# Kernel tuning notes

Measured on AMD Instinct MI355X. Metric: run time of the kernel, lower is better.

The kernel has to match this reference:

```python
import jax, jax.numpy as jnp
import numpy as np

NUM_FEATURES = 512
NUM_HEADS = 8
DIM_PER_HEAD = NUM_FEATURES // NUM_HEADS


def setup_inputs() -> dict:
    key = jax.random.key(0)
    ks = jax.random.split(key, 9)
    B, C, H, W = 8, NUM_FEATURES, 32, 32
    # xavier_uniform bound for 1x1 conv: sqrt(6/(fan_in+fan_out)) = sqrt(6/(2C))
    bound = float(np.sqrt(6.0 / (2.0 * C)))
    # conv bias default init: U(-1/sqrt(fan_in), 1/sqrt(fan_in))
    bbound = float(1.0 / np.sqrt(C))
    return {
        "query": jax.random.normal(ks[0], (B, C, H, W), jnp.float32),
        "key": jax.random.normal(ks[1], (B, C, H, W), jnp.float32),
        "value": jax.random.normal(ks[2], (B, C, H, W), jnp.float32),
        "wq": jax.random.uniform(ks[3], (C, C), jnp.float32, -bound, bound),
        "bq": jax.random.uniform(ks[4], (C,), jnp.float32, -bbound, bbound),
        "wk": jax.random.uniform(ks[5], (C, C), jnp.float32, -bound, bound),
        "bk": jax.random.uniform(ks[6], (C,), jnp.float32, -bbound, bbound),
        "wv": jax.random.uniform(ks[7], (C, C), jnp.float32, -bound, bound),
        "bv": jax.random.uniform(ks[8], (C,), jnp.float32, -bbound, bbound),
    }


def _proj(x, w, b):
    # 1x1 conv == per-pixel linear over channels. x: [B,C,H,W], w: [Cout,Cin]
    return jnp.einsum('oi,bihw->bohw', w, x) + b[None, :, None, None]


def _split_heads(x, nh, d):
    B, C, H, W = x.shape
    # view (B, nh, d, H*W) then permute -> (B, nh, S, d)
    return x.reshape(B, nh, d, H * W).transpose(0, 1, 3, 2)


def reference(query, key, value, wq, bq, wk, bk, wv, bv):
    B, C, H, W = query.shape
    nh, d = NUM_HEADS, DIM_PER_HEAD
    q = _split_heads(_proj(query, wq, bq), nh, d)   # [B,nh,S,d]
    k = _split_heads(_proj(key, wk, bk), nh, d)
    v = _split_heads(_proj(value, wv, bv), nh, d)
    scores = jnp.einsum('bhsd,bhtd->bhst', q, k) / jnp.sqrt(jnp.float32(d))
    attn = jax.nn.softmax(scores, axis=-1)          # [B,nh,S,S]
    out = jnp.einsum('bhst,bhtd->bhsd', attn, v)    # [B,nh,S,d]
    # combine_heads (faithful to torch): permute to (B,S,nh,d), flat reshape
    out = out.transpose(0, 2, 1, 3)                 # [B,S,nh,d]
    return out.reshape(B, C, H, W)
```

## Files before the change

kernel.cpp:

```cpp
#include <hip/hip_runtime.h>
#include <hip/hip_bf16.h>
#include <stdint.h>


typedef __attribute__((ext_vector_type(4))) float f32x4;
typedef __attribute__((ext_vector_type(8))) short short8;
typedef __attribute__((ext_vector_type(4))) unsigned int u32x4;

#define GLB_AS(p) ((const __attribute__((address_space(1))) void*)(p))
#define LDS_AS(p) ((__attribute__((address_space(3))) void*)(p))

__device__ __forceinline__ unsigned short f2b(float f) {
  unsigned int x = __builtin_bit_cast(unsigned int, f);
  x = (x + 0x7FFFu + ((x >> 16) & 1u)) >> 16;
  return (unsigned short)x;
}

__device__ __forceinline__ float exp2_hw(float x) {
  float r;
  asm("v_exp_f32 %0, %1" : "=v"(r) : "v"(x));
  return r;
}

__device__ __forceinline__ unsigned int cvtpk(float lo, float hi) {
  unsigned int r;
  asm("v_cvt_pk_bf16_f32 %0, %1, %2" : "=v"(r) : "v"(lo), "v"(hi));
  return r;
}

__device__ __forceinline__ f32x4 mfma16(short8 a, short8 b, f32x4 c) {
  return __builtin_amdgcn_mfma_f32_16x16x32_bf16(a, b, c, 0, 0, 0);
}

__global__ __launch_bounds__(256) void transpose_cast3(const float* __restrict__ Xq,
                                                       const float* __restrict__ Xk,
                                                       const float* __restrict__ Xv,
                                                       unsigned short* __restrict__ Xt) {
  __shared__ float t[64][65];
  const int which = blockIdx.z >> 3, bb = blockIdx.z & 7;
  const float* X = (which == 0) ? Xq : ((which == 1) ? Xk : Xv);
  const int s0 = blockIdx.x * 64, c0 = blockIdx.y * 64;
  const float* Xb = X + (long)bb * 512 * 1024;
  const int tid = threadIdx.x;
  const int col4 = (tid & 15) * 4;
  const int r0 = tid >> 4;
#pragma unroll
  for (int it = 0; it < 4; ++it) {
    int r = r0 + it * 16;
    const float4 v = *(const float4*)&Xb[(long)(c0 + r) * 1024 + s0 + col4];
    t[r][col4 + 0] = v.x; t[r][col4 + 1] = v.y; t[r][col4 + 2] = v.z; t[r][col4 + 3] = v.w;
  }
  __syncthreads();
  const int s = tid >> 2;
  const int cp = (tid & 3) * 16;
  unsigned int u[8];
#pragma unroll
  for (int i = 0; i < 8; ++i) {
    unsigned int lo = f2b(t[cp + 2 * i][s]);
    unsigned int hi = f2b(t[cp + 2 * i + 1][s]);
    u[i] = lo | (hi << 16);
  }
  unsigned short* dst = Xt + (long)which * 8 * 1024 * 512 +
                        ((long)bb * 1024 + s0 + s) * 512 + c0 + cp;
  ((uint4*)dst)[0] = make_uint4(u[0], u[1], u[2], u[3]);
  ((uint4*)dst)[1] = make_uint4(u[4], u[5], u[6], u[7]);
}

__global__ __launch_bounds__(256) void cast_w3(const float* __restrict__ wq,
                                               const float* __restrict__ wk,
                                               const float* __restrict__ wv,
                                               unsigned short* __restrict__ O) {
  const int y = blockIdx.y;
  const float* W = (y == 0) ? wq : ((y == 1) ? wk : wv);
  int i = blockIdx.x * 256 + threadIdx.x;
  float4 v = ((const float4*)W)[i];
  uint2 u;
  u.x = (unsigned)f2b(v.x) | ((unsigned)f2b(v.y) << 16);
  u.y = (unsigned)f2b(v.z) | ((unsigned)f2b(v.w) << 16);
  ((uint2*)(O + (long)y * 262144))[i] = u;
}

__global__ __launch_bounds__(256, 2) void gemm_proj(
    const unsigned short* __restrict__ XT, const unsigned short* __restrict__ W3,
    unsigned short* __restrict__ QKV, const float* __restrict__ bq,
    const float* __restrict__ bk, const float* __restrict__ bv) {
  __shared__ __align__(16) unsigned short lA[128 * 64];
  __shared__ __align__(16) unsigned short lB[128 * 64];
  const long SC = 1024L * 512;
  const int bid = blockIdx.x;
  const int kind = bid >> 8;
  const int rr = bid & 255;
  const int batch = rr >> 5, tile = rr & 31;
  const unsigned short *Ab, *Bb;
  unsigned short* Cb;
  const float* bias;
  int m0, n0, N, biasN;
  float scale = 1.0f;
  if (kind < 2) {
    m0 = (tile >> 2) * 128; n0 = (tile & 3) * 128; N = 512; biasN = 1;
    Ab = XT + ((long)kind * 8 + batch) * SC;
    Bb = W3 + (long)kind * 262144;
    Cb = QKV + ((long)kind * 8 + batch) * SC;
    bias = kind ? bk : bq;
    if (kind == 0) scale = 0.18033688011112042f;
  } else {
    m0 = (tile >> 3) * 128; n0 = (tile & 7) * 128; N = 1024; biasN = 0;
    Ab = W3 + 2 * 262144;
    Bb = XT + (16L + batch) * SC;
    Cb = QKV + (16L + batch) * SC;
    bias = bv;
  }
  const int tid = threadIdx.x, lane = tid & 63, wid = tid >> 6;
  const int wr = wid >> 1, wc = wid & 1;
  const int lm = lane & 15, lg = lane >> 4;
  f32x4 acc[4][4] = {};
  for (int k0 = 0; k0 < 512; k0 += 64) {
#pragma unroll
    for (int ch = wid; ch < 16; ch += 4) {
      int e = ch * 512 + lane * 8;
      int r = e >> 6, cc = e & 63;
      __builtin_amdgcn_global_load_lds(GLB_AS(Ab + (long)(m0 + r) * 512 + k0 + cc),
                                       LDS_AS(lA + ch * 512), 16, 0, 0);
      __builtin_amdgcn_global_load_lds(GLB_AS(Bb + (long)(n0 + r) * 512 + k0 + cc),
                                       LDS_AS(lB + ch * 512), 16, 0, 0);
    }
    __syncthreads();
#pragma unroll
    for (int kk = 0; kk < 2; ++kk) {
      short8 af[4], bf[4];
#pragma unroll
      for (int i = 0; i < 4; ++i)
        af[i] = *(const short8*)&lA[(wr * 64 + i * 16 + lm) * 64 + kk * 32 + 8 * lg];
#pragma unroll
      for (int j = 0; j < 4; ++j)
        bf[j] = *(const short8*)&lB[(wc * 64 + j * 16 + lm) * 64 + kk * 32 + 8 * lg];
#pragma unroll
      for (int i = 0; i < 4; ++i)
#pragma unroll
        for (int j = 0; j < 4; ++j)
          acc[i][j] = mfma16(af[i], bf[j], acc[i][j]);
    }
    __syncthreads();
  }
#pragma unroll
  for (int i = 0; i < 4; ++i)
#pragma unroll
    for (int j = 0; j < 4; ++j)
#pragma unroll
      for (int r = 0; r < 4; ++r) {
        int m = m0 + wr * 64 + i * 16 + lg * 4 + r;
        int n = n0 + wc * 64 + j * 16 + lm;
        float bvv = biasN ? bias[n] : bias[m];
        Cb[(long)m * N + n] = f2b((acc[i][j][r] + bvv) * scale);
      }
}

__global__ __launch_bounds__(256, 2) void attn(
    const unsigned short* __restrict__ Qt, const unsigned short* __restrict__ Kt,
    const unsigned short* __restrict__ V, float* __restrict__ Out) {
  __shared__ __align__(16) unsigned short lK[2][64 * 64];
  __shared__ __align__(16) unsigned short lV[2][64 * 64];
  const int flat = blockIdx.x;
  const int xcd = flat & 7, j = flat >> 3;
  const int pair = xcd * 8 + (j >> 3);
  const int st = j & 7;
  const int b = pair >> 3, h = pair & 7;
  const int tid = threadIdx.x, lane = tid & 63, w = tid >> 6;
  const int lm = lane & 15, lg = lane >> 4;
  const int s0 = st * 128 + w * 32;
  const unsigned short* Qb = Qt + ((long)b * 1024 + s0) * 512 + h * 64;
  const unsigned short* Kb = Kt + (long)b * 1024 * 512 + h * 64;
  const unsigned short* Vb = V + ((long)b * 512 + h * 64) * 1024;

  const int srow = (w << 1) * 8 + (lane >> 3);
  const int scol = ((lane & 7) ^ (lane >> 3)) * 8;
  auto stage = [&](int buf, int t0) {
#pragma unroll
    for (int jj = 0; jj < 2; ++jj) {
      int ch = (w << 1) + jj;
      int row = srow + jj * 8;
      __builtin_amdgcn_global_load_lds(GLB_AS(Kb + (long)(t0 + row) * 512 + scol),
                                       LDS_AS(&lK[buf][ch * 512]), 16, 0, 0);
      __builtin_amdgcn_global_load_lds(GLB_AS(Vb + (long)row * 1024 + t0 + scol),
                                       LDS_AS(&lV[buf][ch * 512]), 16, 0, 0);
    }
  };

  short8 qf[2][2];
#pragma unroll
  for (int si = 0; si < 2; ++si)
#pragma unroll
    for (int kk = 0; kk < 2; ++kk)
      qf[si][kk] = *(const short8*)&Qb[(si * 16 + lm) * 512 + kk * 32 + 8 * lg];

  f32x4 o[2][4] = {};
  float lsum[2] = {};

  stage(0, 0);
  __syncthreads();

#pragma unroll 1
  for (int t = 0; t < 16; ++t) {
    const int cur = t & 1;
    if (t < 15) stage(cur ^ 1, (t + 1) * 64);
    f32x4 s[2][4] = {};
    __builtin_amdgcn_s_setprio(1);
#pragma unroll
    for (int tj = 0; tj < 4; ++tj) {
      short8 kf0 = *(const short8*)&lK[cur][(tj * 16 + lm) * 64 + 8 * (lg ^ (lm & 7))];
      short8 kf1 = *(const short8*)&lK[cur][(tj * 16 + lm) * 64 + 8 * ((lg + 4) ^ (lm & 7))];
#pragma unroll
      for (int si = 0; si < 2; ++si) {
        s[si][tj] = mfma16(kf0, qf[si][0], s[si][tj]);
        s[si][tj] = mfma16(kf1, qf[si][1], s[si][tj]);
      }
    }
    __builtin_amdgcn_s_setprio(0);
#pragma unroll
    for (int si = 0; si < 2; ++si)
#pragma unroll
      for (int tj = 0; tj < 4; ++tj)
#pragma unroll
        for (int r = 0; r < 4; ++r) {
          float p = exp2_hw(s[si][tj][r]);
          s[si][tj][r] = p;
          lsum[si] += p;
        }
#pragma unroll
    for (int tk = 0; tk < 2; ++tk) {
      short8 pa[2];
#pragma unroll
      for (int si = 0; si < 2; ++si) {
        unsigned int X01 = cvtpk(s[si][2 * tk][0], s[si][2 * tk][1]);
        unsigned int X23 = cvtpk(s[si][2 * tk][2], s[si][2 * tk][3]);
        unsigned int Y01 = cvtpk(s[si][2 * tk + 1][0], s[si][2 * tk + 1][1]);
        unsigned int Y23 = cvtpk(s[si][2 * tk + 1][2], s[si][2 * tk + 1][3]);
        asm("v_permlane32_swap_b32 %0, %1" : "+v"(X01), "+v"(Y01));
        asm("v_permlane32_swap_b32 %0, %1" : "+v"(X23), "+v"(Y23));
        unsigned int Xs01 = (unsigned)__builtin_amdgcn_ds_swizzle((int)X01, 0x401F);
        unsigned int Xs23 = (unsigned)__builtin_amdgcn_ds_swizzle((int)X23, 0x401F);
        unsigned int Ys01 = (unsigned)__builtin_amdgcn_ds_swizzle((int)Y01, 0x401F);
        unsigned int Ys23 = (unsigned)__builtin_amdgcn_ds_swizzle((int)Y23, 0x401F);
        const bool b0 = (lane >> 4) & 1;
        u32x4 pw;
        pw[0] = b0 ? Ys01 : X01;
        pw[1] = b0 ? Ys23 : X23;
        pw[2] = b0 ? Y01 : Xs01;
        pw[3] = b0 ? Y23 : Xs23;
        pa[si] = __builtin_bit_cast(short8, pw);
      }
      __builtin_amdgcn_s_setprio(1);
#pragma unroll
      for (int dj = 0; dj < 4; ++dj) {
        short8 vf = *(const short8*)&lV[cur][(dj * 16 + lm) * 64 + 8 * ((tk * 4 + lg) ^ (lm & 7))];
        o[0][dj] = mfma16(pa[0], vf, o[0][dj]);
        o[1][dj] = mfma16(pa[1], vf, o[1][dj]);
      }
      __builtin_amdgcn_s_setprio(0);
    }
    __syncthreads();
  }

  float inv[2][4];
#pragma unroll
  for (int si = 0; si < 2; ++si) {
    float rs = lsum[si];
    rs += __shfl_xor(rs, 16);
    rs += __shfl_xor(rs, 32);
#pragma unroll
    for (int r = 0; r < 4; ++r)
      inv[si][r] = 1.0f / __shfl(rs, lg * 4 + r);
  }
#pragma unroll
  for (int si = 0; si < 2; ++si)
#pragma unroll
    for (int dj = 0; dj < 4; ++dj)
#pragma unroll
      for (int r = 0; r < 4; ++r) {
        int srow2 = s0 + si * 16 + lg * 4 + r;
        Out[((long)b * 1024 + srow2) * 512 + h * 64 + dj * 16 + lm] = o[si][dj][r] * inv[si][r];
      }
}

extern "C" void kernel_launch(void* const* d_in, const int* in_sizes, int n_in,
                              void* d_out, int out_size, void* d_ws, size_t ws_size,
                              hipStream_t stream) {
  const float* query = (const float*)d_in[0];
  const float* key   = (const float*)d_in[1];
  const float* value = (const float*)d_in[2];
  const float* wq = (const float*)d_in[3];
  const float* bq = (const float*)d_in[4];
  const float* wk = (const float*)d_in[5];
  const float* bk = (const float*)d_in[6];
  const float* wv = (const float*)d_in[7];
  const float* bv = (const float*)d_in[8];

  unsigned short* ws = (unsigned short*)d_ws;
  const long SC = 1024L * 512;
  unsigned short* XT  = ws;
  unsigned short* W3  = XT + 24 * SC;
  unsigned short* QKV = W3 + 3 * 262144;
  unsigned short* QT  = QKV;
  unsigned short* KTm = QKV + 8 * SC;
  unsigned short* VVm = QKV + 16 * SC;

  transpose_cast3<<<dim3(16, 8, 24), 256, 0, stream>>>(query, key, value, XT);
  cast_w3<<<dim3(256, 3), 256, 0, stream>>>(wq, wk, wv, W3);
  gemm_proj<<<768, 256, 0, stream>>>(XT, W3, QKV, bq, bk, bv);
  attn<<<512, 256, 0, stream>>>(QT, KTm, VVm, (float*)d_out);
}
```

Baseline: 69.40 us.

## Split attention key loop across two wave groups and merge partials in LDS

The attention block grows from 4 to 8 waves. Each half of the waves handles half of the 1024 keys with its own double-buffered K/V LDS tiles, so the serial key loop drops from 16 steps to 8. Partial output accumulators and row sums from the second half are written to LDS, reused from the K/V buffers, and added into the first half's values before normalisation and the store. The aim is more latency hiding per CU and a shorter critical path, at the cost of twice the LDS per block and an extra barrier and LDS round trip for the merge.

```diff
diff --git a/kernel.cpp b/kernel.cpp
--- a/kernel.cpp
+++ b/kernel.cpp
@@ -155,34 +155,36 @@
       }
 }
 
-__global__ __launch_bounds__(256, 2) void attn(
+__global__ __launch_bounds__(512, 4) void attn(
     const unsigned short* __restrict__ Qt, const unsigned short* __restrict__ Kt,
     const unsigned short* __restrict__ V, float* __restrict__ Out) {
-  __shared__ __align__(16) unsigned short lK[2][64 * 64];
-  __shared__ __align__(16) unsigned short lV[2][64 * 64];
+  __shared__ __align__(16) unsigned short lK[2][2][64 * 64];
+  __shared__ __align__(16) unsigned short lV[2][2][64 * 64];
   const int flat = blockIdx.x;
   const int xcd = flat & 7, j = flat >> 3;
   const int pair = xcd * 8 + (j >> 3);
   const int st = j & 7;
   const int b = pair >> 3, h = pair & 7;
   const int tid = threadIdx.x, lane = tid & 63, w = tid >> 6;
+  const int half = w >> 2, wq = w & 3;
   const int lm = lane & 15, lg = lane >> 4;
-  const int s0 = st * 128 + w * 32;
+  const int s0 = st * 128 + wq * 32;
+  const int tbase = half * 512;
   const unsigned short* Qb = Qt + ((long)b * 1024 + s0) * 512 + h * 64;
   const unsigned short* Kb = Kt + (long)b * 1024 * 512 + h * 64;
   const unsigned short* Vb = V + ((long)b * 512 + h * 64) * 1024;
 
-  const int srow = (w << 1) * 8 + (lane >> 3);
+  const int srow = (wq << 1) * 8 + (lane >> 3);
   const int scol = ((lane & 7) ^ (lane >> 3)) * 8;
   auto stage = [&](int buf, int t0) {
 #pragma unroll
     for (int jj = 0; jj < 2; ++jj) {
-      int ch = (w << 1) + jj;
+      int ch = (wq << 1) + jj;
       int row = srow + jj * 8;
       __builtin_amdgcn_global_load_lds(GLB_AS(Kb + (long)(t0 + row) * 512 + scol),
-                                       LDS_AS(&lK[buf][ch * 512]), 16, 0, 0);
+                                       LDS_AS(&lK[half][buf][ch * 512]), 16, 0, 0);
       __builtin_amdgcn_global_load_lds(GLB_AS(Vb + (long)row * 1024 + t0 + scol),
-                                       LDS_AS(&lV[buf][ch * 512]), 16, 0, 0);
+                                       LDS_AS(&lV[half][buf][ch * 512]), 16, 0, 0);
     }
   };
 
@@ -196,19 +198,19 @@
   f32x4 o[2][4] = {};
   float lsum[2] = {};
 
-  stage(0, 0);
+  stage(0, tbase);
   __syncthreads();
 
 #pragma unroll 1
-  for (int t = 0; t < 16; ++t) {
+  for (int t = 0; t < 8; ++t) {
     const int cur = t & 1;
-    if (t < 15) stage(cur ^ 1, (t + 1) * 64);
+    if (t < 7) stage(cur ^ 1, tbase + (t + 1) * 64);
     f32x4 s[2][4] = {};
     __builtin_amdgcn_s_setprio(1);
 #pragma unroll
     for (int tj = 0; tj < 4; ++tj) {
-      short8 kf0 = *(const short8*)&lK[cur][(tj * 16 + lm) * 64 + 8 * (lg ^ (lm & 7))];
-      short8 kf1 = *(const short8*)&lK[cur][(tj * 16 + lm) * 64 + 8 * ((lg + 4) ^ (lm & 7))];
+      short8 kf0 = *(const short8*)&lK[half][cur][(tj * 16 + lm) * 64 + 8 * (lg ^ (lm & 7))];
+      short8 kf1 = *(const short8*)&lK[half][cur][(tj * 16 + lm) * 64 + 8 * ((lg + 4) ^ (lm & 7))];
 #pragma unroll
       for (int si = 0; si < 2; ++si) {
         s[si][tj] = mfma16(kf0, qf[si][0], s[si][tj]);
@@ -252,7 +254,7 @@
       __builtin_amdgcn_s_setprio(1);
 #pragma unroll
       for (int dj = 0; dj < 4; ++dj) {
-        short8 vf = *(const short8*)&lV[cur][(dj * 16 + lm) * 64 + 8 * ((tk * 4 + lg) ^ (lm & 7))];
+        short8 vf = *(const short8*)&lV[half][cur][(dj * 16 + lm) * 64 + 8 * ((tk * 4 + lg) ^ (lm & 7))];
         o[0][dj] = mfma16(pa[0], vf, o[0][dj]);
         o[1][dj] = mfma16(pa[1], vf, o[1][dj]);
       }
@@ -261,25 +263,50 @@
     __syncthreads();
   }
 
-  float inv[2][4];
-#pragma unroll
-  for (int si = 0; si < 2; ++si) {
-    float rs = lsum[si];
-    rs += __shfl_xor(rs, 16);
-    rs += __shfl_xor(rs, 32);
-#pragma unroll
-    for (int r = 0; r < 4; ++r)
-      inv[si][r] = 1.0f / __shfl(rs, lg * 4 + r);
-  }
-#pragma unroll
-  for (int si = 0; si < 2; ++si)
-#pragma unroll
-    for (int dj = 0; dj < 4; ++dj)
-#pragma unroll
-      for (int r = 0; r < 4; ++r) {
-        int srow2 = s0 + si * 16 + lg * 4 + r;
-        Out[((long)b * 1024 + srow2) * 512 + h * 64 + dj * 16 + lm] = o[si][dj][r] * inv[si][r];
-      }
+  float* exO = (float*)&lK[0][0][0];
+  float* exL = (float*)&lV[0][0][0];
+  if (half) {
+#pragma unroll
+    for (int si = 0; si < 2; ++si) {
+      exL[(wq * 2 + si) * 64 + lane] = lsum[si];
+#pragma unroll
+      for (int dj = 0; dj < 4; ++dj)
+#pragma unroll
+        for (int r = 0; r < 4; ++r)
+          exO[(wq * 32 + si * 16 + lg * 4 + r) * 64 + dj * 16 + lm] = o[si][dj][r];
+    }
+  }
+  __syncthreads();
+  if (!half) {
+#pragma unroll
+    for (int si = 0; si < 2; ++si) {
+      lsum[si] += exL[(wq * 2 + si) * 64 + lane];
+#pragma unroll
+      for (int dj = 0; dj < 4; ++dj)
+#pragma unroll
+        for (int r = 0; r < 4; ++r)
+          o[si][dj][r] += exO[(wq * 32 + si * 16 + lg * 4 + r) * 64 + dj * 16 + lm];
+    }
+    float inv[2][4];
+#pragma unroll
+    for (int si = 0; si < 2; ++si) {
+      float rs = lsum[si];
+      rs += __shfl_xor(rs, 16);
+      rs += __shfl_xor(rs, 32);
+#pragma unroll
+      for (int r = 0; r < 4; ++r)
+        inv[si][r] = 1.0f / __shfl(rs, lg * 4 + r);
+    }
+#pragma unroll
+    for (int si = 0; si < 2; ++si)
+#pragma unroll
+      for (int dj = 0; dj < 4; ++dj)
+#pragma unroll
+        for (int r = 0; r < 4; ++r) {
+          int srow2 = s0 + si * 16 + lg * 4 + r;
+          Out[((long)b * 1024 + srow2) * 512 + h * 64 + dj * 16 + lm] = o[si][dj][r] * inv[si][r];
+        }
+  }
 }
 
 extern "C" void kernel_launch(void* const* d_in, const int* in_sizes, int n_in,
@@ -307,5 +334,5 @@
   transpose_cast3<<<dim3(16, 8, 24), 256, 0, stream>>>(query, key, value, XT);
   cast_w3<<<dim3(256, 3), 256, 0, stream>>>(wq, wk, wv, W3);
   gemm_proj<<<768, 256, 0, stream>>>(XT, W3, QKV, bq, bk, bv);
-  attn<<<512, 256, 0, stream>>>(QT, KTm, VVm, (float*)d_out);
-}
+  attn<<<512, 512, 0, stream>>>(QT, KTm, VVm, (float*)d_out);
+}
```

Result: no change. 69.17 us (-0.3%).

## Triple-buffer K/V tiles with partial vmcnt waits and use permlane16 swap

Applied to the files above, without the earlier changes.

Moves the attention kernel's K/V staging from double to triple buffering. Loads are issued two tiles ahead, and the per-iteration __syncthreads is replaced by an explicit vmcnt(4) wait plus s_barrier, so one tile's loads stay in flight across the barrier. It also replaces four ds_swizzle ops and lane selects with v_permlane16_swap when building the P operand. LDS use grows by half, which may limit occupancy at two blocks per CU, and the counted waits depend on the exact number of outstanding loads.

```diff
diff --git a/kernel.cpp b/kernel.cpp
--- a/kernel.cpp
+++ b/kernel.cpp
@@ -158,8 +158,8 @@
 __global__ __launch_bounds__(256, 2) void attn(
     const unsigned short* __restrict__ Qt, const unsigned short* __restrict__ Kt,
     const unsigned short* __restrict__ V, float* __restrict__ Out) {
-  __shared__ __align__(16) unsigned short lK[2][64 * 64];
-  __shared__ __align__(16) unsigned short lV[2][64 * 64];
+  __shared__ __align__(16) unsigned short lK[3][64 * 64];
+  __shared__ __align__(16) unsigned short lV[3][64 * 64];
   const int flat = blockIdx.x;
   const int xcd = flat & 7, j = flat >> 3;
   const int pair = xcd * 8 + (j >> 3);
@@ -197,12 +197,15 @@
   float lsum[2] = {};
 
   stage(0, 0);
-  __syncthreads();
+  stage(1, 64);
+  asm volatile("s_waitcnt vmcnt(4) lgkmcnt(0)" ::: "memory");
+  __builtin_amdgcn_s_barrier();
+  __builtin_amdgcn_sched_barrier(0);
 
 #pragma unroll 1
   for (int t = 0; t < 16; ++t) {
-    const int cur = t & 1;
-    if (t < 15) stage(cur ^ 1, (t + 1) * 64);
+    const int cur = t % 3;
+    if (t < 14) stage((t + 2) % 3, (t + 2) * 64);
     f32x4 s[2][4] = {};
     __builtin_amdgcn_s_setprio(1);
 #pragma unroll
@@ -237,16 +240,13 @@
         unsigned int Y23 = cvtpk(s[si][2 * tk + 1][2], s[si][2 * tk + 1][3]);
         asm("v_permlane32_swap_b32 %0, %1" : "+v"(X01), "+v"(Y01));
         asm("v_permlane32_swap_b32 %0, %1" : "+v"(X23), "+v"(Y23));
-        unsigned int Xs01 = (unsigned)__builtin_amdgcn_ds_swizzle((int)X01, 0x401F);
-        unsigned int Xs23 = (unsigned)__builtin_amdgcn_ds_swizzle((int)X23, 0x401F);
-        unsigned int Ys01 = (unsigned)__builtin_amdgcn_ds_swizzle((int)Y01, 0x401F);
-        unsigned int Ys23 = (unsigned)__builtin_amdgcn_ds_swizzle((int)Y23, 0x401F);
-        const bool b0 = (lane >> 4) & 1;
+        asm("v_permlane16_swap_b32 %0, %1" : "+v"(X01), "+v"(Y01));
+        asm("v_permlane16_swap_b32 %0, %1" : "+v"(X23), "+v"(Y23));
         u32x4 pw;
-        pw[0] = b0 ? Ys01 : X01;
-        pw[1] = b0 ? Ys23 : X23;
-        pw[2] = b0 ? Y01 : Xs01;
-        pw[3] = b0 ? Y23 : Xs23;
+        pw[0] = X01;
+        pw[1] = X23;
+        pw[2] = Y01;
+        pw[3] = Y23;
         pa[si] = __builtin_bit_cast(short8, pw);
       }
       __builtin_amdgcn_s_setprio(1);
@@ -258,7 +258,15 @@
       }
       __builtin_amdgcn_s_setprio(0);
     }
-    __syncthreads();
+    if (t < 14) {
+      asm volatile("s_waitcnt vmcnt(4) lgkmcnt(0)" ::: "memory");
+      __builtin_amdgcn_s_barrier();
+      __builtin_amdgcn_sched_barrier(0);
+    } else if (t == 14) {
+      asm volatile("s_waitcnt vmcnt(0) lgkmcnt(0)" ::: "memory");
+      __builtin_amdgcn_s_barrier();
+      __builtin_amdgcn_sched_barrier(0);
+    }
   }
 
   float inv[2][4];
```

After: 69.02 us. No clear change (-0.6%).
